# Kernel tuning notes

Measured on AMD Instinct MI355X. Metric: run time of the kernel, lower is better.

The kernel has to match this reference:

```python
import jax, jax.numpy as jnp
import numpy as np

# --- geometry constants (ProtoDUNE-HD-like) ---
B, F, T = 1, 1, 256            # batch, input features, nticks
NCHANS = 2560                   # total readout channels (800+800+480+480)
NWIRES = [800, 800, 480]        # wires per plane (U, V, W) on each face
NCELLS = 40000                  # number of 3-wire crossing cells per face
MLP_HID, MLP_OUT = 8, 2

# channel ranges per (face, plane): induction planes (U,V) wrap both faces,
# collection (W) channels are disjoint per face
_CHAN_RANGES = {(0, 0): (0, 800), (0, 1): (800, 1600), (0, 2): (1600, 2080),
                (1, 0): (0, 800), (1, 1): (800, 1600), (1, 2): (2080, 2560)}


def _make_tables():
    rng = np.random.default_rng(0)
    wcs = {}
    for (f, p), (lo, hi) in _CHAN_RANGES.items():
        n = hi - lo
        ch = lo + rng.permutation(n)                       # irregular wire->channel map
        wcs[(f, p)] = np.stack([np.arange(n), ch], axis=1).astype(np.int64)
    gi = {}
    for f in (0, 1):
        gi[f] = np.stack([rng.integers(0, NWIRES[p], NCELLS) for p in range(3)],
                         axis=1).astype(np.int64)          # (NCELLS, 3) wire idx per plane
    return wcs, gi


def setup_inputs() -> dict:
    key = jax.random.key(0)
    k = jax.random.split(key, 5)
    wcs, gi = _make_tables()
    inp = {
        'x':  jax.random.normal(k[0], (B, F, NCHANS, T), jnp.float32),
        'W1': jax.random.normal(k[1], (3 * F, MLP_HID), jnp.float32) * 0.5,
        'b1': jax.random.normal(k[2], (MLP_HID,), jnp.float32) * 0.1,
        'W2': jax.random.normal(k[3], (MLP_HID, MLP_OUT), jnp.float32) * 0.5,
        'b2': jax.random.normal(k[4], (MLP_OUT,), jnp.float32) * 0.1,
        'gi0': jnp.asarray(gi[0]), 'gi1': jnp.asarray(gi[1]),
    }
    for f in (0, 1):
        for p in range(3):
            inp[f'wc{f}{p}'] = jnp.asarray(wcs[(f, p)])
    return inp


def _make_wires(x, wc):
    # wires[..., wire_ident, :] = x[..., channel, :]   (Network.make_wires)
    Bb, Ff, _, Tt = x.shape
    wires = jnp.zeros((Bb, Ff, wc.shape[0], Tt), x.dtype)
    return wires.at[:, :, wc[:, 0], :].set(x[:, :, wc[:, 1], :])


def _crossview_mlp(x, W1, b1, W2, b2, wcs, gis):
    # mp_step: relu -> per-face cross-view gather -> MLP -> amax scatter -> concat
    x = jax.nn.relu(x)
    Bb, Ff, C, Tt = x.shape
    scattered = jnp.zeros((Bb, MLP_OUT, C, Tt), x.dtype)   # zeros init => amax includes 0
    for f in range(2):
        gi = gis[f]
        # gather the three plane views for each crossing cell: (B, 3F, NCELLS, T)
        cells = jnp.concatenate(
            [_make_wires(x, wcs[f][p])[:, :, gi[:, p], :] for p in range(3)], axis=1)
        h = jnp.einsum('bfnt,fh->bhnt', cells, W1) + b1[None, :, None, None]
        y = jnp.einsum('bhnt,ho->bont', h, W2) + b2[None, :, None, None]
        # scatter_to_chans: amax-reduce cell outputs back onto readout channels
        for p in range(3):
            ch = wcs[f][p][gi[:, p], 1]                    # channel of each cell's wire
            scattered = scattered.at[:, :, ch, :].max(y)
    # special_style == 'mlp': concat input features with cross-view MLP features
    return jnp.concatenate([x, scattered], axis=1)         # (B, F+MLP_OUT, C, T)


def reference(x, W1, b1, W2, b2, wc00, wc01, wc02, wc10, wc11, wc12, gi0, gi1):
    wcs = ((wc00, wc01, wc02), (wc10, wc11, wc12))
    gis = (gi0, gi1)
    return _crossview_mlp(x, W1, b1, W2, b2, wcs, gis)
```

## Files before the change

### kernel.cpp

```cpp
#include <hip/hip_runtime.h>
#include <hip/hip_fp16.h>

#define NCHANS 2560
#define TT 256
#define NCELLS_ 40000
#define NINST 240000
#define HALF_NINST 120000
#define CAP 192

#define WS_CURSOR 0
#define WS_XR     16384
#define WS_EPACK  1327104

#define PREP_BLOCKS 640
#define FILL_BLOCKS 938

__device__ __forceinline__ __half2 pk_max_f16(__half2 a, __half2 b) {
    unsigned int ua = *(unsigned int*)&a;
    unsigned int ub = *(unsigned int*)&b;
    unsigned int ur;
    asm("v_pk_max_f16 %0, %1, %2" : "=v"(ur) : "v"(ua), "v"(ub));
    return *(__half2*)&ur;
}

__global__ __launch_bounds__(256) void prep_fill_kernel(
    const float* __restrict__ x,
    const int* __restrict__ gi0, const int* __restrict__ gi1,
    const int* __restrict__ wc00, const int* __restrict__ wc01, const int* __restrict__ wc02,
    const int* __restrict__ wc10, const int* __restrict__ wc11, const int* __restrict__ wc12,
    int* __restrict__ cursor, uint2* __restrict__ epack, uint2* __restrict__ xr,
    float* __restrict__ out)
{
    const int b = blockIdx.x;
    if (b < PREP_BLOCKS) {
        const int i = b * 256 + threadIdx.x;
        float4 v = ((const float4*)x)[i];
        v.x = fmaxf(v.x, 0.f); v.y = fmaxf(v.y, 0.f);
        v.z = fmaxf(v.z, 0.f); v.w = fmaxf(v.w, 0.f);
        ((float4*)out)[i] = v;
        __half2 h01 = __floats2half2_rn(v.x, v.y);
        __half2 h23 = __floats2half2_rn(v.z, v.w);
        uint2 p;
        p.x = *(unsigned int*)&h01;
        p.y = *(unsigned int*)&h23;
        xr[i] = p;
    } else {
        const int j = (b - PREP_BLOCKS) * 256 + threadIdx.x;
        if (j >= NINST) return;
        const int face = (j >= HALF_NINST) ? 1 : 0;
        const int i = j - face * HALF_NINST;
        const int p = i % 3;
        const int cellBase = i - p;
        const int* gi = face ? gi1 : gi0;
        const int w0 = gi[cellBase + 0];
        const int w1 = gi[cellBase + 1];
        const int w2 = gi[cellBase + 2];
        const int* wcA = face ? wc10 : wc00;
        const int* wcB = face ? wc11 : wc01;
        const int* wcC = face ? wc12 : wc02;
        const int c0 = wcA[w0 * 2 + 1];
        const int c1 = wcB[w1 * 2 + 1];
        const int c2 = wcC[w2 * 2 + 1];
        const int cOwn = (p == 0) ? c0 : ((p == 1) ? c1 : c2);
        uint2 E;
        E.x = (unsigned)c0 | ((unsigned)c1 << 16);
        E.y = (unsigned)c2;
        const int s = atomicAdd(&cursor[cOwn], 1);
        if (s < CAP) epack[cOwn * CAP + s] = E;
    }
}

__global__ __launch_bounds__(256) void gather_kernel(
    const float* __restrict__ W1, const float* __restrict__ b1,
    const float* __restrict__ W2, const float* __restrict__ b2,
    const int* __restrict__ cursor, const uint2* __restrict__ epack,
    const char* __restrict__ xr, float* __restrict__ out)
{
    float A[3][2], C[2];
#pragma unroll
    for (int o = 0; o < 2; ++o) {
        float s = b2[o];
#pragma unroll
        for (int h = 0; h < 8; ++h) s += b1[h] * W2[h * 2 + o];
        C[o] = s;
    }
#pragma unroll
    for (int p = 0; p < 3; ++p)
#pragma unroll
        for (int o = 0; o < 2; ++o) {
            float s = 0.f;
#pragma unroll
            for (int h = 0; h < 8; ++h) s += W1[p * 8 + h] * W2[h * 2 + o];
            A[p][o] = s;
        }
    __half2 a2[3][2], C2[2];
#pragma unroll
    for (int p = 0; p < 3; ++p)
#pragma unroll
        for (int o = 0; o < 2; ++o) a2[p][o] = __half2half2(__float2half(A[p][o]));
    C2[0] = __half2half2(__float2half(C[0]));
    C2[1] = __half2half2(__float2half(C[1]));

    const int w = threadIdx.x >> 6;
    const int lane = threadIdx.x & 63;
    const int wid = blockIdx.x * 4 + w;
    int ch = wid >> 1;
    const int half = wid & 1;
    ch = __builtin_amdgcn_readfirstlane(ch);

    int n = cursor[ch];
    n = n < CAP ? n : CAP;
    const uint2* ep = epack + ch * CAP;
    const char* base = xr + half * 256 + lane * 4;

    __half2 m0 = __half2half2(__float2half(0.f));
    __half2 m1 = m0;

#pragma unroll 2
    for (int e = 0; e < n; ++e) {
        const uint2 E = ep[e];
        const int c0 = E.x & 0xFFFFu;
        const int c1 = E.x >> 16;
        const int c2 = E.y;
        const __half2 f0 = *(const __half2*)(base + (c0 << 9));
        const __half2 f1 = *(const __half2*)(base + (c1 << 9));
        const __half2 f2 = *(const __half2*)(base + (c2 << 9));
        const __half2 y0 = __hfma2(a2[0][0], f0, __hfma2(a2[1][0], f1, __hfma2(a2[2][0], f2, C2[0])));
        const __half2 y1 = __hfma2(a2[0][1], f0, __hfma2(a2[1][1], f1, __hfma2(a2[2][1], f2, C2[1])));
        m0 = pk_max_f16(m0, y0);
        m1 = pk_max_f16(m1, y1);
    }

    const int off = ch * TT + half * 128 + lane * 2;
    float2* o1 = (float2*)(out + NCHANS * TT + off);
    float2* o2 = (float2*)(out + 2 * NCHANS * TT + off);
    *o1 = make_float2(__low2float(m0), __high2float(m0));
    *o2 = make_float2(__low2float(m1), __high2float(m1));
}

extern "C" void kernel_launch(void* const* d_in, const int* in_sizes, int n_in,
                              void* d_out, int out_size, void* d_ws, size_t ws_size,
                              hipStream_t stream) {
    const float* x  = (const float*)d_in[0];
    const float* W1 = (const float*)d_in[1];
    const float* b1 = (const float*)d_in[2];
    const float* W2 = (const float*)d_in[3];
    const float* b2 = (const float*)d_in[4];
    const int* gi0  = (const int*)d_in[5];
    const int* gi1  = (const int*)d_in[6];
    const int* wc00 = (const int*)d_in[7];
    const int* wc01 = (const int*)d_in[8];
    const int* wc02 = (const int*)d_in[9];
    const int* wc10 = (const int*)d_in[10];
    const int* wc11 = (const int*)d_in[11];
    const int* wc12 = (const int*)d_in[12];
    float* out = (float*)d_out;

    char* ws = (char*)d_ws;
    int*   cursor = (int*)(ws + WS_CURSOR);
    uint2* xr     = (uint2*)(ws + WS_XR);
    uint2* epack  = (uint2*)(ws + WS_EPACK);

    (void)hipMemsetAsync(cursor, 0, NCHANS * sizeof(int), stream);

    prep_fill_kernel<<<PREP_BLOCKS + FILL_BLOCKS, 256, 0, stream>>>(
        x, gi0, gi1, wc00, wc01, wc02, wc10, wc11, wc12,
        cursor, epack, xr, out);

    gather_kernel<<<NCHANS * 2 / 4, 256, 0, stream>>>(
        W1, b1, W2, b2, cursor, epack, (const char*)xr, out);
}
```

Baseline: 76.74 us.

## Fuse memset, prep/fill and gather into one cooperative kernel with grid syncs

Replaces the memset plus two kernel launches with a single cooperative kernel of 640 blocks. It zeroes the cursors, runs prep and the bucket fill, then does the gather, with grid-wide syncs between phases. The gather now gives one wave per channel covering all 256 ticks with 8-byte loads. Cell entries are staged through shared memory in chunks of 64. This removes launch and memset overhead at the cost of two grid barriers and lower parallelism in the fill and gather phases.

```diff
diff --git a/kernel.cpp b/kernel.cpp
--- a/kernel.cpp
+++ b/kernel.cpp
@@ -1,19 +1,21 @@
 #include <hip/hip_runtime.h>
 #include <hip/hip_fp16.h>
+#include <hip/hip_cooperative_groups.h>
+
+namespace cg = cooperative_groups;
 
 #define NCHANS 2560
 #define TT 256
-#define NCELLS_ 40000
 #define NINST 240000
 #define HALF_NINST 120000
 #define CAP 192
+#define NBLK 640
+#define NTHR 256
+#define NITEM 163840
 
 #define WS_CURSOR 0
 #define WS_XR     16384
 #define WS_EPACK  1327104
-
-#define PREP_BLOCKS 640
-#define FILL_BLOCKS 938
 
 __device__ __forceinline__ __half2 pk_max_f16(__half2 a, __half2 b) {
     unsigned int ua = *(unsigned int*)&a;
@@ -22,31 +24,38 @@
     asm("v_pk_max_f16 %0, %1, %2" : "=v"(ur) : "v"(ua), "v"(ub));
     return *(__half2*)&ur;
 }
+__device__ __forceinline__ __half2 u2h(unsigned int u) { return *(__half2*)&u; }
 
-__global__ __launch_bounds__(256) void prep_fill_kernel(
+__global__ __launch_bounds__(256) void fused_kernel(
     const float* __restrict__ x,
+    const float* __restrict__ W1, const float* __restrict__ b1,
+    const float* __restrict__ W2, const float* __restrict__ b2,
     const int* __restrict__ gi0, const int* __restrict__ gi1,
     const int* __restrict__ wc00, const int* __restrict__ wc01, const int* __restrict__ wc02,
     const int* __restrict__ wc10, const int* __restrict__ wc11, const int* __restrict__ wc12,
     int* __restrict__ cursor, uint2* __restrict__ epack, uint2* __restrict__ xr,
     float* __restrict__ out)
 {
-    const int b = blockIdx.x;
-    if (b < PREP_BLOCKS) {
-        const int i = b * 256 + threadIdx.x;
-        float4 v = ((const float4*)x)[i];
+    cg::grid_group grid = cg::this_grid();
+    const int tid = blockIdx.x * NTHR + threadIdx.x;
+
+    if (tid < NCHANS) cursor[tid] = 0;
+    grid.sync();
+
+    {
+        float4 v = ((const float4*)x)[tid];
         v.x = fmaxf(v.x, 0.f); v.y = fmaxf(v.y, 0.f);
         v.z = fmaxf(v.z, 0.f); v.w = fmaxf(v.w, 0.f);
-        ((float4*)out)[i] = v;
+        ((float4*)out)[tid] = v;
         __half2 h01 = __floats2half2_rn(v.x, v.y);
         __half2 h23 = __floats2half2_rn(v.z, v.w);
         uint2 p;
         p.x = *(unsigned int*)&h01;
         p.y = *(unsigned int*)&h23;
-        xr[i] = p;
-    } else {
-        const int j = (b - PREP_BLOCKS) * 256 + threadIdx.x;
-        if (j >= NINST) return;
+        xr[tid] = p;
+    }
+
+    for (int j = tid; j < NINST; j += NBLK * NTHR) {
         const int face = (j >= HALF_NINST) ? 1 : 0;
         const int i = j - face * HALF_NINST;
         const int p = i % 3;
@@ -68,74 +77,75 @@
         const int s = atomicAdd(&cursor[cOwn], 1);
         if (s < CAP) epack[cOwn * CAP + s] = E;
     }
-}
+    grid.sync();
 
-__global__ __launch_bounds__(256) void gather_kernel(
-    const float* __restrict__ W1, const float* __restrict__ b1,
-    const float* __restrict__ W2, const float* __restrict__ b2,
-    const int* __restrict__ cursor, const uint2* __restrict__ epack,
-    const char* __restrict__ xr, float* __restrict__ out)
-{
-    float A[3][2], C[2];
-#pragma unroll
-    for (int o = 0; o < 2; ++o) {
-        float s = b2[o];
-#pragma unroll
-        for (int h = 0; h < 8; ++h) s += b1[h] * W2[h * 2 + o];
-        C[o] = s;
-    }
-#pragma unroll
-    for (int p = 0; p < 3; ++p)
+    {
+        float Af[3][2], Cf[2];
 #pragma unroll
         for (int o = 0; o < 2; ++o) {
-            float s = 0.f;
+            float s = b2[o];
 #pragma unroll
-            for (int h = 0; h < 8; ++h) s += W1[p * 8 + h] * W2[h * 2 + o];
-            A[p][o] = s;
+            for (int h = 0; h < 8; ++h) s += b1[h] * W2[h * 2 + o];
+            Cf[o] = s;
         }
-    __half2 a2[3][2], C2[2];
 #pragma unroll
-    for (int p = 0; p < 3; ++p)
+        for (int p = 0; p < 3; ++p)
 #pragma unroll
-        for (int o = 0; o < 2; ++o) a2[p][o] = __half2half2(__float2half(A[p][o]));
-    C2[0] = __half2half2(__float2half(C[0]));
-    C2[1] = __half2half2(__float2half(C[1]));
+            for (int o = 0; o < 2; ++o) {
+                float s = 0.f;
+#pragma unroll
+                for (int h = 0; h < 8; ++h) s += W1[p * 8 + h] * W2[h * 2 + o];
+                Af[p][o] = s;
+            }
+        __half2 a2[3][2], C2[2];
+#pragma unroll
+        for (int p = 0; p < 3; ++p)
+#pragma unroll
+            for (int o = 0; o < 2; ++o) a2[p][o] = __half2half2(__float2half(Af[p][o]));
+        C2[0] = __half2half2(__float2half(Cf[0]));
+        C2[1] = __half2half2(__float2half(Cf[1]));
 
-    const int w = threadIdx.x >> 6;
-    const int lane = threadIdx.x & 63;
-    const int wid = blockIdx.x * 4 + w;
-    int ch = wid >> 1;
-    const int half = wid & 1;
-    ch = __builtin_amdgcn_readfirstlane(ch);
+        __shared__ uint2 sE[4][64];
+        const int w = threadIdx.x >> 6;
+        const int lane = threadIdx.x & 63;
+        int ch = blockIdx.x * 4 + w;
+        ch = __builtin_amdgcn_readfirstlane(ch);
 
-    int n = cursor[ch];
-    n = n < CAP ? n : CAP;
-    const uint2* ep = epack + ch * CAP;
-    const char* base = xr + half * 256 + lane * 4;
+        int n = cursor[ch];
+        n = n < CAP ? n : CAP;
+        const uint2* ep = epack + ch * CAP;
+        const char* xrb = (const char*)xr + lane * 8;
 
-    __half2 m0 = __half2half2(__float2half(0.f));
-    __half2 m1 = m0;
+        __half2 m00 = __half2half2(__float2half(0.f));
+        __half2 m01 = m00, m10 = m00, m11 = m00;
 
-#pragma unroll 2
-    for (int e = 0; e < n; ++e) {
-        const uint2 E = ep[e];
-        const int c0 = E.x & 0xFFFFu;
-        const int c1 = E.x >> 16;
-        const int c2 = E.y;
-        const __half2 f0 = *(const __half2*)(base + (c0 << 9));
-        const __half2 f1 = *(const __half2*)(base + (c1 << 9));
-        const __half2 f2 = *(const __half2*)(base + (c2 << 9));
-        const __half2 y0 = __hfma2(a2[0][0], f0, __hfma2(a2[1][0], f1, __hfma2(a2[2][0], f2, C2[0])));
-        const __half2 y1 = __hfma2(a2[0][1], f0, __hfma2(a2[1][1], f1, __hfma2(a2[2][1], f2, C2[1])));
-        m0 = pk_max_f16(m0, y0);
-        m1 = pk_max_f16(m1, y1);
+        for (int base = 0; base < n; base += 64) {
+            int k = n - base; k = k > 64 ? 64 : k;
+            if (lane < k) sE[w][lane] = ep[base + lane];
+#pragma unroll 4
+            for (int e = 0; e < k; ++e) {
+                const uint2 E = sE[w][e];
+                const int c0 = E.x & 0xFFFFu;
+                const int c1 = E.x >> 16;
+                const int c2 = E.y;
+                const uint2 d0 = *(const uint2*)(xrb + (c0 << 9));
+                const uint2 d1 = *(const uint2*)(xrb + (c1 << 9));
+                const uint2 d2 = *(const uint2*)(xrb + (c2 << 9));
+                const __half2 y0a = __hfma2(a2[0][0], u2h(d0.x), __hfma2(a2[1][0], u2h(d1.x), __hfma2(a2[2][0], u2h(d2.x), C2[0])));
+                const __half2 y0b = __hfma2(a2[0][0], u2h(d0.y), __hfma2(a2[1][0], u2h(d1.y), __hfma2(a2[2][0], u2h(d2.y), C2[0])));
+                const __half2 y1a = __hfma2(a2[0][1], u2h(d0.x), __hfma2(a2[1][1], u2h(d1.x), __hfma2(a2[2][1], u2h(d2.x), C2[1])));
+                const __half2 y1b = __hfma2(a2[0][1], u2h(d0.y), __hfma2(a2[1][1], u2h(d1.y), __hfma2(a2[2][1], u2h(d2.y), C2[1])));
+                m00 = pk_max_f16(m00, y0a); m01 = pk_max_f16(m01, y0b);
+                m10 = pk_max_f16(m10, y1a); m11 = pk_max_f16(m11, y1b);
+            }
+        }
+
+        const int off = ch * TT + lane * 4;
+        *(float4*)(out + NCHANS * TT + off) =
+            make_float4(__low2float(m00), __high2float(m00), __low2float(m01), __high2float(m01));
+        *(float4*)(out + 2 * NCHANS * TT + off) =
+            make_float4(__low2float(m10), __high2float(m10), __low2float(m11), __high2float(m11));
     }
-
-    const int off = ch * TT + half * 128 + lane * 2;
-    float2* o1 = (float2*)(out + NCHANS * TT + off);
-    float2* o2 = (float2*)(out + 2 * NCHANS * TT + off);
-    *o1 = make_float2(__low2float(m0), __high2float(m0));
-    *o2 = make_float2(__low2float(m1), __high2float(m1));
 }
 
 extern "C" void kernel_launch(void* const* d_in, const int* in_sizes, int n_in,
@@ -161,12 +171,11 @@
     uint2* xr     = (uint2*)(ws + WS_XR);
     uint2* epack  = (uint2*)(ws + WS_EPACK);
 
-    (void)hipMemsetAsync(cursor, 0, NCHANS * sizeof(int), stream);
-
-    prep_fill_kernel<<<PREP_BLOCKS + FILL_BLOCKS, 256, 0, stream>>>(
-        x, gi0, gi1, wc00, wc01, wc02, wc10, wc11, wc12,
-        cursor, epack, xr, out);
-
-    gather_kernel<<<NCHANS * 2 / 4, 256, 0, stream>>>(
-        W1, b1, W2, b2, cursor, epack, (const char*)xr, out);
+    void* args[] = { (void*)&x, (void*)&W1, (void*)&b1, (void*)&W2, (void*)&b2,
+                     (void*)&gi0, (void*)&gi1,
+                     (void*)&wc00, (void*)&wc01, (void*)&wc02,
+                     (void*)&wc10, (void*)&wc11, (void*)&wc12,
+                     (void*)&cursor, (void*)&epack, (void*)&xr, (void*)&out };
+    (void)hipLaunchCooperativeKernel((const void*)fused_kernel,
+                                     dim3(NBLK), dim3(NTHR), args, 0, stream);
 }
```

Result: slower. 198.8 us (+159.1%).
